# Kernel optimization log

Hardware: AMD Instinct MI355X
Metric: run time of the kernel (lower is better)

The kernel has to match this reference:

```python
import jax, jax.numpy as jnp
import numpy as np
import math

B, S, D = 2, 8192, 1024
NW, SHIFT = 16, 256          # num_windows, shift_window
NH, DH = 16, 64              # heads = D // dim_head
DFF = 4 * D
EPS = 1e-6


def setup_inputs() -> dict:
    key = jax.random.key(0)
    ks = jax.random.split(key, 12)
    s = 1.0 / math.sqrt(D)
    return {
        "x": jax.random.normal(ks[0], (B, S, D), jnp.float32),
        "wq": jax.random.normal(ks[1], (D, NH * DH), jnp.float32) * s,
        "wk": jax.random.normal(ks[2], (D, NH * DH), jnp.float32) * s,
        "wv": jax.random.normal(ks[3], (D, NH * DH), jnp.float32) * s,
        "wo": jax.random.normal(ks[4], (NH * DH, D), jnp.float32) * s,
        "g_attn": jnp.ones((D,), jnp.float32),
        "g_ff": jnp.ones((D,), jnp.float32),
        "w1": jax.random.normal(ks[5], (D, DFF), jnp.float32) * s,
        "b1": jnp.zeros((DFF,), jnp.float32),
        "w2": jax.random.normal(ks[6], (DFF, D), jnp.float32) * (1.0 / math.sqrt(DFF)),
        "b2": jnp.zeros((D,), jnp.float32),
    }


def _rmsnorm(x, g):
    return x * g * jax.lax.rsqrt(jnp.mean(x * x, axis=-1, keepdims=True) + EPS)


def reference(x, wq, wk, wv, wo, g_attn, g_ff, w1, b1, w2, b2):
    skip = x
    h = _rmsnorm(x, g_attn)
    # shift (note: source rolls by -shift both before AND after attention)
    h = jnp.roll(h, -SHIFT, axis=1)
    # window partition: [B, NW, n, D]
    n = S // NW
    h = h.reshape(B, NW, n, D)
    q = (h @ wq).reshape(B, NW, n, NH, DH)
    k = (h @ wk).reshape(B, NW, n, NH, DH)
    v = (h @ wv).reshape(B, NW, n, NH, DH)
    scores = jnp.einsum('bwqhd,bwkhd->bwhqk', q, k) * (1.0 / math.sqrt(DH))
    a = jax.nn.softmax(scores, axis=-1)
    o = jnp.einsum('bwhqk,bwkhd->bwqhd', a, v).reshape(B, NW, n, NH * DH)
    o = (o @ wo).reshape(B, S, D)
    o = jnp.roll(o, -SHIFT, axis=1)  # faithful to source (rolls -shift again)
    x = o + skip
    skip = x
    h = _rmsnorm(x, g_ff)
    h = jax.nn.gelu(h @ w1 + b1) @ w2 + b2
    return h + skip
```

## Files before the change

### kernel.cpp

```cpp
#include <hip/hip_runtime.h>
#include <stdint.h>

#define S_LEN 8192
#define D_DIM 1024
#define SHIFT_W 256
#define NROWS 16384

typedef __bf16 bf16;
typedef __bf16 bf16x8 __attribute__((ext_vector_type(8)));
typedef __bf16 bf16x4 __attribute__((ext_vector_type(4)));
typedef float f32x4 __attribute__((ext_vector_type(4)));

typedef __attribute__((address_space(1))) const void gas_t;
typedef __attribute__((address_space(3))) void las_t;

__device__ __forceinline__ void load_lds16(const void* g, void* l) {
  __builtin_amdgcn_global_load_lds((gas_t*)g, (las_t*)l, 16, 0, 0);
}

__device__ __forceinline__ int xcd_swizzle(int orig, int nwg) {
  return (orig & 7) * (nwg >> 3) + (orig >> 3);
}

__global__ __launch_bounds__(256) void k_transpose_cvt(const float* __restrict__ in,
                                                       bf16* __restrict__ out,
                                                       int R, int C) {
  __shared__ float tile[32][33];
  int lx = threadIdx.x & 31, ly = threadIdx.x >> 5;
  int tc = blockIdx.x * 32, tr = blockIdx.y * 32;
#pragma unroll
  for (int i = 0; i < 4; i++)
    tile[ly + i * 8][lx] = in[(size_t)(tr + ly + i * 8) * C + tc + lx];
  __syncthreads();
#pragma unroll
  for (int i = 0; i < 4; i++)
    out[(size_t)(tc + ly + i * 8) * R + tr + lx] = (bf16)tile[lx][ly + i * 8];
}

__global__ __launch_bounds__(256) void k_rmsnorm(const float* __restrict__ x,
                                                 const float* __restrict__ g,
                                                 bf16* __restrict__ out, int shift) {
  int row = blockIdx.x;
  int b = row >> 13, r = row & (S_LEN - 1);
  int src = (b << 13) | ((r + shift) & (S_LEN - 1));
  int t = threadIdx.x;
  float4 v = *(const float4*)(x + (size_t)src * D_DIM + t * 4);
  float ss = v.x * v.x + v.y * v.y + v.z * v.z + v.w * v.w;
#pragma unroll
  for (int off = 32; off; off >>= 1) ss += __shfl_xor(ss, off);
  __shared__ float red[4];
  if ((t & 63) == 0) red[t >> 6] = ss;
  __syncthreads();
  ss = red[0] + red[1] + red[2] + red[3];
  float sc = rsqrtf(ss * (1.0f / D_DIM) + 1e-6f);
  float4 gv = *(const float4*)(g + t * 4);
  bf16x4 o;
  o[0] = (bf16)(v.x * gv.x * sc);
  o[1] = (bf16)(v.y * gv.y * sc);
  o[2] = (bf16)(v.z * gv.z * sc);
  o[3] = (bf16)(v.w * gv.w * sc);
  *(bf16x4*)(out + (size_t)row * D_DIM + t * 4) = o;
}

template <int EPI>
__global__ __launch_bounds__(256, 3) void k_gemm(const bf16* __restrict__ A,
                                                 const bf16* __restrict__ BT,
                                                 bf16* __restrict__ obf,
                                                 float* __restrict__ of32,
                                                 const float* __restrict__ bias,
                                                 const float* __restrict__ skip,
                                                 int K, int ldc) {
  __shared__ __align__(16) char smem[32768];
  const int tid = threadIdx.x;
  const int wv = tid >> 6, lane = tid & 63;
  const int lr = lane & 15, lg = lane >> 4;
  const int wr = (wv >> 1) * 64, wc = (wv & 1) * 64;

  const int NB = gridDim.x >> 7;
  const int xcd = blockIdx.x & 7;
  const int l = blockIdx.x >> 3;
  const int mb = ((xcd & 3) << 5) + (l & 31);
  const int nb = (xcd >> 2) * (NB >> 1) + (l >> 5);
  const int m0 = mb * 128, n0 = nb * 128;

  const int srow = tid >> 3;
  const int scolb = ((tid & 7) ^ (srow & 7)) << 4;
  const bf16* gA = A + (size_t)(m0 + srow) * K + (scolb >> 1);
  const bf16* gB = BT + (size_t)(n0 + srow) * K + (scolb >> 1);
  char* lA = smem + wv * 1024;
  char* lB = smem + 16384 + wv * 1024;

  f32x4 acc[4][4] = {};

  for (int k0 = 0; k0 < K; k0 += 64) {
    __syncthreads();
#pragma unroll
    for (int i = 0; i < 4; i++) {
      load_lds16(gA + (size_t)(i * 32) * K + k0, lA + i * 4096);
      load_lds16(gB + (size_t)(i * 32) * K + k0, lB + i * 4096);
    }
    __syncthreads();
#pragma unroll
    for (int kk = 0; kk < 2; kk++) {
      bf16x8 af[4], bff[4];
#pragma unroll
      for (int i = 0; i < 4; i++) {
        int ra = wr + i * 16 + lr;
        af[i] = *(const bf16x8*)(smem + ra * 128 + ((kk * 64 + lg * 16) ^ ((ra & 7) << 4)));
        int rb = wc + i * 16 + lr;
        bff[i] = *(const bf16x8*)(smem + 16384 + rb * 128 + ((kk * 64 + lg * 16) ^ ((rb & 7) << 4)));
      }
      __builtin_amdgcn_s_setprio(1);
#pragma unroll
      for (int mi = 0; mi < 4; mi++)
#pragma unroll
        for (int ni = 0; ni < 4; ni++)
          acc[mi][ni] = __builtin_amdgcn_mfma_f32_16x16x32_bf16(af[mi], bff[ni], acc[mi][ni], 0, 0, 0);
      __builtin_amdgcn_s_setprio(0);
    }
  }

  float* lds_f = (float*)smem;
  const int erow = tid >> 2;
  const int ecol0 = (tid & 3) * 16;
#pragma unroll
  for (int w = 0; w < 4; w++) {
    __syncthreads();
    if (wv == w) {
#pragma unroll
      for (int mf = 0; mf < 4; mf++) {
        int lrow = mf * 16 + lg * 4;
#pragma unroll
        for (int nf = 0; nf < 4; nf++) {
          int lcol = nf * 16 + lr;
#pragma unroll
          for (int ii = 0; ii < 4; ii++)
            lds_f[(lrow + ii) * 66 + lcol] = acc[mf][nf][ii];
        }
      }
    }
    __syncthreads();
    int gr = m0 + (w >> 1) * 64 + erow;
    size_t orow;
    if constexpr (EPI == 1) {
      int b = gr >> 13, rr = gr & (S_LEN - 1);
      orow = (size_t)((b << 13) | ((rr - SHIFT_W) & (S_LEN - 1))) * ldc;
    } else {
      orow = (size_t)gr * ldc;
    }
    int col0 = n0 + (w & 1) * 64 + ecol0;
#pragma unroll
    for (int j = 0; j < 4; j++) {
      f32x4 v = *(const f32x4*)&lds_f[erow * 66 + ecol0 + j * 4];
      int col = col0 + j * 4;
      if constexpr (EPI == 0) {
        bf16x4 o;
#pragma unroll
        for (int e = 0; e < 4; e++) o[e] = (bf16)v[e];
        *(bf16x4*)(obf + orow + col) = o;
      } else if constexpr (EPI == 1) {
        f32x4 s = *(const f32x4*)(skip + orow + col);
        f32x4 r = v + s;
        *(f32x4*)(of32 + orow + col) = r;
      } else if constexpr (EPI == 2) {
        f32x4 bi = *(const f32x4*)(bias + col);
        bf16x4 o;
#pragma unroll
        for (int e = 0; e < 4; e++) {
          float z = v[e] + bi[e];
          float u = 0.7978845608f * (z + 0.044715f * z * z * z);
          u = fminf(fmaxf(u, -15.f), 15.f);
          float ex = __expf(2.f * u);
          o[e] = (bf16)(0.5f * z * (1.f + (ex - 1.f) / (ex + 1.f)));
        }
        *(bf16x4*)(obf + orow + col) = o;
      } else {
        f32x4 bi = *(const f32x4*)(bias + col);
        f32x4 s = *(const f32x4*)(skip + orow + col);
        f32x4 r = v + bi + s;
        *(f32x4*)(of32 + orow + col) = r;
      }
    }
  }
}

__global__ __launch_bounds__(256) void k_attn(const bf16* __restrict__ qkv,
                                              bf16* __restrict__ out) {
  __shared__ __align__(16) char Qs[8192];
  __shared__ __align__(16) char Ks[8192];
  __shared__ __align__(16) char Vs[8192];
  __shared__ __align__(16) char Ps[4][2048];
  const int tid = threadIdx.x;
  const int wave = tid >> 6, lane = tid & 63;
  const int lr = lane & 15, lg = lane >> 4;
  const int bid = xcd_swizzle(blockIdx.x, gridDim.x);
  const int qt = bid & 7;
  const int h = (bid >> 3) & 15;
  const int bw = bid >> 7;
  const int rowbase = bw * 512;
  const int qrow0 = rowbase + qt * 64;

  {
    int r = tid >> 2, c0 = tid & 3;
    const bf16* src = qkv + (size_t)(qrow0 + r) * 3072 + h * 64;
#pragma unroll
    for (int j = 0; j < 2; j++) {
      int ch = c0 + j * 4;
      uint4 val = *(const uint4*)(src + ch * 8);
      int byte = (r * 128 + ch * 16) ^ ((r & 7) << 4);
      *(uint4*)(Qs + byte) = val;
    }
  }
  __syncthreads();
  bf16x8 qf[2];
  {
    int qr = wave * 16 + lr;
#pragma unroll
    for (int kk = 0; kk < 2; kk++) {
      int byte = (qr * 128 + (kk * 32 + lg * 8) * 2) ^ ((qr & 7) << 4);
      qf[kk] = *(const bf16x8*)(Qs + byte);
    }
  }

  f32x4 oacc[4] = {};
  float m_run = -__builtin_inff(), l_run = 0.f;

  for (int kt = 0; kt < 8; ++kt) {
    __syncthreads();
    {
      int r = tid >> 2, c0 = tid & 3;
      const bf16* ksrc = qkv + (size_t)(rowbase + kt * 64 + r) * 3072 + 1024 + h * 64;
      const bf16* vsrc = ksrc + 1024;
#pragma unroll
      for (int j = 0; j < 2; j++) {
        int ch = c0 + j * 4;
        uint4 val = *(const uint4*)(ksrc + ch * 8);
        int byte = (r * 128 + ch * 16) ^ ((r & 7) << 4);
        *(uint4*)(Ks + byte) = val;
      }
#pragma unroll
      for (int j = 0; j < 2; j++) {
        int ch = c0 + j * 4;
        bf16x8 vv = *(const bf16x8*)(vsrc + ch * 8);
#pragma unroll
        for (int e = 0; e < 8; e++) {
          int d = ch * 8 + e;
          int byte = (d * 128 + r * 2) ^ ((d & 7) << 4);
          *(bf16*)(Vs + byte) = vv[e];
        }
      }
    }
    __syncthreads();
    f32x4 sc[4] = {};
#pragma unroll
    for (int kk = 0; kk < 2; kk++)
#pragma unroll
      for (int mf = 0; mf < 4; mf++) {
        int kr = mf * 16 + lr;
        int byte = (kr * 128 + (kk * 32 + lg * 8) * 2) ^ ((kr & 7) << 4);
        bf16x8 kf = *(const bf16x8*)(Ks + byte);
        sc[mf] = __builtin_amdgcn_mfma_f32_16x16x32_bf16(kf, qf[kk], sc[mf], 0, 0, 0);
      }
    float mx = -__builtin_inff();
#pragma unroll
    for (int mf = 0; mf < 4; mf++)
#pragma unroll
      for (int i = 0; i < 4; i++) mx = fmaxf(mx, sc[mf][i]);
    mx = fmaxf(mx, __shfl_xor(mx, 16));
    mx = fmaxf(mx, __shfl_xor(mx, 32));
    float mnew = fmaxf(m_run, mx);
    float alpha = __expf(0.125f * (m_run - mnew));
    float lsum = 0.f;
    float ps[4][4];
#pragma unroll
    for (int mf = 0; mf < 4; mf++)
#pragma unroll
      for (int i = 0; i < 4; i++) {
        float p = __expf(0.125f * (sc[mf][i] - mnew));
        ps[mf][i] = p;
        lsum += p;
      }
    lsum += __shfl_xor(lsum, 16);
    lsum += __shfl_xor(lsum, 32);
    l_run = l_run * alpha + lsum;
    m_run = mnew;
#pragma unroll
    for (int dm = 0; dm < 4; dm++) oacc[dm] *= alpha;
#pragma unroll
    for (int mf = 0; mf < 4; mf++) {
      bf16x4 pv;
#pragma unroll
      for (int i = 0; i < 4; i++) pv[i] = (bf16)ps[mf][i];
      int byte = (lr * 128 + (mf * 16 + lg * 4) * 2) ^ ((lr & 7) << 4);
      *(bf16x4*)(Ps[wave] + byte) = pv;
    }
#pragma unroll
    for (int kk = 0; kk < 2; kk++) {
      int pbyte = (lr * 128 + (kk * 32 + lg * 8) * 2) ^ ((lr & 7) << 4);
      bf16x8 pf = *(const bf16x8*)(Ps[wave] + pbyte);
#pragma unroll
      for (int dm = 0; dm < 4; dm++) {
        int d = dm * 16 + lr;
        int byte = (d * 128 + (kk * 32 + lg * 8) * 2) ^ ((d & 7) << 4);
        bf16x8 vf = *(const bf16x8*)(Vs + byte);
        oacc[dm] = __builtin_amdgcn_mfma_f32_16x16x32_bf16(vf, pf, oacc[dm], 0, 0, 0);
      }
    }
  }
  float inv = 1.f / l_run;
  int rowq = qrow0 + wave * 16 + lr;
#pragma unroll
  for (int dm = 0; dm < 4; dm++) {
    bf16x4 ov;
#pragma unroll
    for (int i = 0; i < 4; i++) ov[i] = (bf16)(oacc[dm][i] * inv);
    *(bf16x4*)(out + (size_t)rowq * 1024 + h * 64 + dm * 16 + lg * 4) = ov;
  }
}

extern "C" void kernel_launch(void* const* d_in, const int* in_sizes, int n_in,
                              void* d_out, int out_size, void* d_ws, size_t ws_size,
                              hipStream_t stream) {
  const float* x = (const float*)d_in[0];
  const float* wq = (const float*)d_in[1];
  const float* wk = (const float*)d_in[2];
  const float* wv = (const float*)d_in[3];
  const float* wo = (const float*)d_in[4];
  const float* ga = (const float*)d_in[5];
  const float* gf = (const float*)d_in[6];
  const float* w1 = (const float*)d_in[7];
  const float* b1 = (const float*)d_in[8];
  const float* w2 = (const float*)d_in[9];
  const float* b2 = (const float*)d_in[10];
  float* out = (float*)d_out;

  char* ws = (char*)d_ws;
  const size_t MB = 1024 * 1024;
  bf16* wqkvT = (bf16*)(ws);
  bf16* woT = (bf16*)(ws + 6 * MB);
  bf16* w1T = (bf16*)(ws + 8 * MB);
  bf16* w2T = (bf16*)(ws + 16 * MB);
  float* x1 = (float*)(ws + 24 * MB);
  bf16* hbuf = (bf16*)(ws + 88 * MB);
  bf16* qkv = (bf16*)(ws + 120 * MB);
  bf16* mid = qkv;

  k_transpose_cvt<<<dim3(32, 32), 256, 0, stream>>>(wq, wqkvT, 1024, 1024);
  k_transpose_cvt<<<dim3(32, 32), 256, 0, stream>>>(wk, wqkvT + 1024 * 1024, 1024, 1024);
  k_transpose_cvt<<<dim3(32, 32), 256, 0, stream>>>(wv, wqkvT + 2 * 1024 * 1024, 1024, 1024);
  k_transpose_cvt<<<dim3(32, 32), 256, 0, stream>>>(wo, woT, 1024, 1024);
  k_transpose_cvt<<<dim3(128, 32), 256, 0, stream>>>(w1, w1T, 1024, 4096);
  k_transpose_cvt<<<dim3(32, 128), 256, 0, stream>>>(w2, w2T, 4096, 1024);

  k_rmsnorm<<<NROWS, 256, 0, stream>>>(x, ga, hbuf, SHIFT_W);
  k_gemm<0><<<128 * 24, 256, 0, stream>>>(hbuf, wqkvT, qkv, nullptr, nullptr, nullptr, 1024, 3072);
  k_attn<<<4096, 256, 0, stream>>>(qkv, hbuf);
  k_gemm<1><<<128 * 8, 256, 0, stream>>>(hbuf, woT, nullptr, x1, nullptr, x, 1024, 1024);
  k_rmsnorm<<<NROWS, 256, 0, stream>>>(x1, gf, hbuf, 0);
  k_gemm<2><<<128 * 32, 256, 0, stream>>>(hbuf, w1T, mid, nullptr, b1, nullptr, 1024, 4096);
  k_gemm<3><<<128 * 8, 256, 0, stream>>>(mid, w2T, nullptr, out, b2, x1, 4096, 1024);
}
```

Before: 727.5 us.

## Enlarge GEMM tiles to 256x128 with 128x64 per-wave subtiles

The GEMM block tile grows from 128x128 to 256x128, so each wave computes 128x64 with 32 accumulators. This raises MFMA work per LDS fragment load and halves the B-operand reloads across blocks. The LDS layout is reorganised into 32-wide k-chunks with a new XOR swizzle, the epilogue is restructured for 128-column staging, and grid sizes are halved to match. In exchange, register and LDS use rise, occupancy drops from 3 to 2 blocks per CU, and there are fewer blocks to fill the 256 CUs on the smaller GEMMs.

```diff
diff --git a/kernel.cpp b/kernel.cpp
--- a/kernel.cpp
+++ b/kernel.cpp
@@ -63,125 +63,135 @@
 }
 
 template <int EPI>
-__global__ __launch_bounds__(256, 3) void k_gemm(const bf16* __restrict__ A,
+__global__ __launch_bounds__(256, 2) void k_gemm(const bf16* __restrict__ A,
                                                  const bf16* __restrict__ BT,
                                                  bf16* __restrict__ obf,
                                                  float* __restrict__ of32,
                                                  const float* __restrict__ bias,
                                                  const float* __restrict__ skip,
                                                  int K, int ldc) {
-  __shared__ __align__(16) char smem[32768];
+  __shared__ __align__(16) char smem[49152];
   const int tid = threadIdx.x;
   const int wv = tid >> 6, lane = tid & 63;
   const int lr = lane & 15, lg = lane >> 4;
-  const int wr = (wv >> 1) * 64, wc = (wv & 1) * 64;
-
-  const int NB = gridDim.x >> 7;
+  const int wm = wv >> 1, wn = wv & 1;
+
+  const int NB = gridDim.x >> 6;
   const int xcd = blockIdx.x & 7;
   const int l = blockIdx.x >> 3;
-  const int mb = ((xcd & 3) << 5) + (l & 31);
-  const int nb = (xcd >> 2) * (NB >> 1) + (l >> 5);
-  const int m0 = mb * 128, n0 = nb * 128;
-
-  const int srow = tid >> 3;
-  const int scolb = ((tid & 7) ^ (srow & 7)) << 4;
-  const bf16* gA = A + (size_t)(m0 + srow) * K + (scolb >> 1);
-  const bf16* gB = BT + (size_t)(n0 + srow) * K + (scolb >> 1);
-  char* lA = smem + wv * 1024;
-  char* lB = smem + 16384 + wv * 1024;
-
-  f32x4 acc[4][4] = {};
+  const int mb = ((xcd & 3) << 4) + (l & 15);
+  const int nb = (xcd >> 2) * (NB >> 1) + (l >> 4);
+  const int m0 = mb * 256, n0 = nb * 128;
+
+  const int r_local = tid >> 2;
+  const int c_src = ((tid & 3) ^ ((r_local >> 1) & 3)) * 8;
+  const bf16* gA = A + (size_t)(m0 + r_local) * K + c_src;
+  const bf16* gB = BT + (size_t)(n0 + r_local) * K + c_src;
+  const int wvbase = wv * 1024;
+
+  const int kchunk = (lg ^ ((lr >> 1) & 3)) << 4;
+  const int aBase = wm * 8192 + lr * 64 + kchunk;
+  const int bBase = 32768 + wn * 4096 + lr * 64 + kchunk;
+
+  f32x4 acc[8][4] = {};
 
   for (int k0 = 0; k0 < K; k0 += 64) {
     __syncthreads();
 #pragma unroll
-    for (int i = 0; i < 4; i++) {
-      load_lds16(gA + (size_t)(i * 32) * K + k0, lA + i * 4096);
-      load_lds16(gB + (size_t)(i * 32) * K + k0, lB + i * 4096);
-    }
+    for (int kc = 0; kc < 2; kc++)
+#pragma unroll
+      for (int g = 0; g < 4; g++)
+        load_lds16(gA + (size_t)(g * 64) * K + k0 + kc * 32,
+                   smem + kc * 16384 + g * 4096 + wvbase);
+#pragma unroll
+    for (int kc = 0; kc < 2; kc++)
+#pragma unroll
+      for (int g = 0; g < 2; g++)
+        load_lds16(gB + (size_t)(g * 64) * K + k0 + kc * 32,
+                   smem + 32768 + kc * 8192 + g * 4096 + wvbase);
     __syncthreads();
 #pragma unroll
-    for (int kk = 0; kk < 2; kk++) {
-      bf16x8 af[4], bff[4];
-#pragma unroll
-      for (int i = 0; i < 4; i++) {
-        int ra = wr + i * 16 + lr;
-        af[i] = *(const bf16x8*)(smem + ra * 128 + ((kk * 64 + lg * 16) ^ ((ra & 7) << 4)));
-        int rb = wc + i * 16 + lr;
-        bff[i] = *(const bf16x8*)(smem + 16384 + rb * 128 + ((kk * 64 + lg * 16) ^ ((rb & 7) << 4)));
-      }
+    for (int kc = 0; kc < 2; kc++) {
+      bf16x8 af[8], bfr[4];
+#pragma unroll
+      for (int mf = 0; mf < 8; mf++)
+        af[mf] = *(const bf16x8*)(smem + kc * 16384 + aBase + mf * 1024);
+#pragma unroll
+      for (int nf = 0; nf < 4; nf++)
+        bfr[nf] = *(const bf16x8*)(smem + kc * 8192 + bBase + nf * 1024);
       __builtin_amdgcn_s_setprio(1);
 #pragma unroll
-      for (int mi = 0; mi < 4; mi++)
-#pragma unroll
-        for (int ni = 0; ni < 4; ni++)
-          acc[mi][ni] = __builtin_amdgcn_mfma_f32_16x16x32_bf16(af[mi], bff[ni], acc[mi][ni], 0, 0, 0);
+      for (int mf = 0; mf < 8; mf++)
+#pragma unroll
+        for (int nf = 0; nf < 4; nf++)
+          acc[mf][nf] = __builtin_amdgcn_mfma_f32_16x16x32_bf16(af[mf], bfr[nf], acc[mf][nf], 0, 0, 0);
       __builtin_amdgcn_s_setprio(0);
     }
   }
 
   float* lds_f = (float*)smem;
   const int erow = tid >> 2;
-  const int ecol0 = (tid & 3) * 16;
-#pragma unroll
-  for (int w = 0; w < 4; w++) {
-    __syncthreads();
-    if (wv == w) {
-#pragma unroll
-      for (int mf = 0; mf < 4; mf++) {
-        int lrow = mf * 16 + lg * 4;
-#pragma unroll
-        for (int nf = 0; nf < 4; nf++) {
-          int lcol = nf * 16 + lr;
-#pragma unroll
-          for (int ii = 0; ii < 4; ii++)
-            lds_f[(lrow + ii) * 66 + lcol] = acc[mf][nf][ii];
+  const int ecol0 = (tid & 3) * 4;
+#pragma unroll
+  for (int wmr = 0; wmr < 2; wmr++)
+#pragma unroll
+    for (int mh = 0; mh < 2; mh++) {
+      __syncthreads();
+      if (wm == wmr) {
+#pragma unroll
+        for (int mf = 0; mf < 4; mf++) {
+          int lrow = mf * 16 + lg * 4;
+#pragma unroll
+          for (int nf = 0; nf < 4; nf++) {
+            int lcol = wn * 64 + nf * 16 + lr;
+#pragma unroll
+            for (int ii = 0; ii < 4; ii++)
+              lds_f[(lrow + ii) * 132 + lcol] = acc[mh * 4 + mf][nf][ii];
+          }
         }
       }
-    }
-    __syncthreads();
-    int gr = m0 + (w >> 1) * 64 + erow;
-    size_t orow;
-    if constexpr (EPI == 1) {
-      int b = gr >> 13, rr = gr & (S_LEN - 1);
-      orow = (size_t)((b << 13) | ((rr - SHIFT_W) & (S_LEN - 1))) * ldc;
-    } else {
-      orow = (size_t)gr * ldc;
-    }
-    int col0 = n0 + (w & 1) * 64 + ecol0;
-#pragma unroll
-    for (int j = 0; j < 4; j++) {
-      f32x4 v = *(const f32x4*)&lds_f[erow * 66 + ecol0 + j * 4];
-      int col = col0 + j * 4;
-      if constexpr (EPI == 0) {
-        bf16x4 o;
-#pragma unroll
-        for (int e = 0; e < 4; e++) o[e] = (bf16)v[e];
-        *(bf16x4*)(obf + orow + col) = o;
-      } else if constexpr (EPI == 1) {
-        f32x4 s = *(const f32x4*)(skip + orow + col);
-        f32x4 r = v + s;
-        *(f32x4*)(of32 + orow + col) = r;
-      } else if constexpr (EPI == 2) {
-        f32x4 bi = *(const f32x4*)(bias + col);
-        bf16x4 o;
-#pragma unroll
-        for (int e = 0; e < 4; e++) {
-          float z = v[e] + bi[e];
-          float u = 0.7978845608f * (z + 0.044715f * z * z * z);
-          u = fminf(fmaxf(u, -15.f), 15.f);
-          float ex = __expf(2.f * u);
-          o[e] = (bf16)(0.5f * z * (1.f + (ex - 1.f) / (ex + 1.f)));
+      __syncthreads();
+      int gr = m0 + wmr * 128 + mh * 64 + erow;
+      size_t orow;
+      if constexpr (EPI == 1) {
+        int b = gr >> 13, rr = gr & (S_LEN - 1);
+        orow = (size_t)((b << 13) | ((rr - SHIFT_W) & (S_LEN - 1))) * ldc;
+      } else {
+        orow = (size_t)gr * ldc;
+      }
+#pragma unroll
+      for (int j = 0; j < 8; j++) {
+        f32x4 v = *(const f32x4*)&lds_f[erow * 132 + ecol0 + j * 16];
+        int col = n0 + ecol0 + j * 16;
+        if constexpr (EPI == 0) {
+          bf16x4 o;
+#pragma unroll
+          for (int e = 0; e < 4; e++) o[e] = (bf16)v[e];
+          *(bf16x4*)(obf + orow + col) = o;
+        } else if constexpr (EPI == 1) {
+          f32x4 s = *(const f32x4*)(skip + orow + col);
+          f32x4 r = v + s;
+          *(f32x4*)(of32 + orow + col) = r;
+        } else if constexpr (EPI == 2) {
+          f32x4 bi = *(const f32x4*)(bias + col);
+          bf16x4 o;
+#pragma unroll
+          for (int e = 0; e < 4; e++) {
+            float z = v[e] + bi[e];
+            float u = 0.7978845608f * (z + 0.044715f * z * z * z);
+            u = fminf(fmaxf(u, -15.f), 15.f);
+            float ex = __expf(2.f * u);
+            o[e] = (bf16)(0.5f * z * (1.f + (ex - 1.f) / (ex + 1.f)));
+          }
+          *(bf16x4*)(obf + orow + col) = o;
+        } else {
+          f32x4 bi = *(const f32x4*)(bias + col);
+          f32x4 s = *(const f32x4*)(skip + orow + col);
+          f32x4 r = v + bi + s;
+          *(f32x4*)(of32 + orow + col) = r;
         }
-        *(bf16x4*)(obf + orow + col) = o;
-      } else {
-        f32x4 bi = *(const f32x4*)(bias + col);
-        f32x4 s = *(const f32x4*)(skip + orow + col);
-        f32x4 r = v + bi + s;
-        *(f32x4*)(of32 + orow + col) = r;
-      }
-    }
-  }
+      }
+    }
 }
 
 __global__ __launch_bounds__(256) void k_attn(const bf16* __restrict__ qkv,
@@ -353,10 +363,10 @@
   k_transpose_cvt<<<dim3(32, 128), 256, 0, stream>>>(w2, w2T, 4096, 1024);
 
   k_rmsnorm<<<NROWS, 256, 0, stream>>>(x, ga, hbuf, SHIFT_W);
-  k_gemm<0><<<128 * 24, 256, 0, stream>>>(hbuf, wqkvT, qkv, nullptr, nullptr, nullptr, 1024, 3072);
+  k_gemm<0><<<64 * 24, 256, 0, stream>>>(hbuf, wqkvT, qkv, nullptr, nullptr, nullptr, 1024, 3072);
   k_attn<<<4096, 256, 0, stream>>>(qkv, hbuf);
-  k_gemm<1><<<128 * 8, 256, 0, stream>>>(hbuf, woT, nullptr, x1, nullptr, x, 1024, 1024);
+  k_gemm<1><<<64 * 8, 256, 0, stream>>>(hbuf, woT, nullptr, x1, nullptr, x, 1024, 1024);
   k_rmsnorm<<<NROWS, 256, 0, stream>>>(x1, gf, hbuf, 0);
-  k_gemm<2><<<128 * 32, 256, 0, stream>>>(hbuf, w1T, mid, nullptr, b1, nullptr, 1024, 4096);
-  k_gemm<3><<<128 * 8, 256, 0, stream>>>(mid, w2T, nullptr, out, b2, x1, 4096, 1024);
-}
+  k_gemm<2><<<64 * 32, 256, 0, stream>>>(hbuf, w1T, mid, nullptr, b1, nullptr, 1024, 4096);
+  k_gemm<3><<<64 * 8, 256, 0, stream>>>(mid, w2T, nullptr, out, b2, x1, 4096, 1024);
+}
```

Result: faster. 684.9 us (-5.9%).
